# Optimization experiments

Hardware: AMD Instinct MI355X
Metric: run time of the kernel (lower is better)

Reference implementation:

```python
import jax, jax.numpy as jnp
import numpy as np
import math

H = 8
D_MODEL = 512
D_K = D_MODEL // H
NEG = -1.0e9


def setup_inputs() -> dict:
    key = jax.random.key(0)
    ks = jax.random.split(key, 10)
    B, S, D = 8, 1024, D_MODEL
    s = 1.0 / math.sqrt(D)
    return {
        "query": jax.random.normal(ks[0], (B, S, D), jnp.float32),
        "key": jax.random.normal(ks[1], (B, S, D), jnp.float32),
        "value": jax.random.normal(ks[2], (B, S, D), jnp.float32),
        "group_prob": jax.random.uniform(ks[3], (B, S, S), jnp.float32),
        "Wq": jax.random.normal(ks[4], (D, D), jnp.float32) * s,
        "Wk": jax.random.normal(ks[5], (D, D), jnp.float32) * s,
        "Wv": jax.random.normal(ks[6], (D, D), jnp.float32) * s,
        "Wh": jax.random.normal(ks[7], (D, D), jnp.float32) * s,
        "bh": jax.random.normal(ks[8], (D,), jnp.float32) * s,
        "mask": jax.random.randint(ks[9], (B, S, S), 0, 2, jnp.int32),
    }


def reference(query, key, value, group_prob, Wq, Wk, Wv, Wh, bh, mask):
    B, S, D = query.shape
    # project and split heads: [B, H, S, d_k]
    def split(x, W):
        return (x @ W.T).reshape(B, S, H, D_K).transpose(0, 2, 1, 3)
    q, k, v = split(query, Wq), split(key, Wk), split(value, Wv)
    scores = jnp.einsum('bhqd,bhkd->bhqk', q, k) / jnp.sqrt(jnp.asarray(D_K, q.dtype))
    # masked_fill where (mask | eye) == 0, i.e. keep mask-allowed or diagonal positions
    eye = jnp.eye(S, dtype=jnp.int32)
    allowed = (mask[:, None, :, :] | eye[None, None, :, :]) != 0  # [B,1,S,S]
    scores = jnp.where(allowed, scores, jnp.asarray(NEG, scores.dtype))
    p_attn = jax.nn.softmax(scores, axis=-1)
    p_attn = p_attn * group_prob[:, None, :, :]  # post-softmax group scaling
    x = jnp.einsum('bhqk,bhkd->bhqd', p_attn, v)
    x = x.transpose(0, 2, 1, 3).reshape(B, S, D)
    return x @ Wh.T + bh
```

## Files before the change

kernel.cpp:

```cpp
#include <hip/hip_runtime.h>
#include <hip/hip_bf16.h>
#include <cstdint>


typedef __attribute__((ext_vector_type(8))) short short8;
typedef __attribute__((ext_vector_type(4))) float f32x4;

__device__ __forceinline__ ushort f2bf(float x) {
    union { __hip_bfloat16 h; ushort u; } v;
    v.h = __float2bfloat16(x);
    return v.u;
}
__device__ __forceinline__ float bf2f(ushort u) {
    union { uint u; float f; } v; v.u = ((uint)u) << 16; return v.f;
}
__device__ __forceinline__ uint cvtpk(float lo, float hi) {
    uint r;
    asm("v_cvt_pk_bf16_f32 %0, %1, %2" : "=v"(r) : "v"(lo), "v"(hi));
    return r;
}
__device__ __forceinline__ f32x4 mfma16(short8 a, short8 b, f32x4 c) {
    return __builtin_amdgcn_mfma_f32_16x16x32_bf16(a, b, c, 0, 0, 0);
}
__device__ __forceinline__ void gl16(const void* g, const void* l) {
    __builtin_amdgcn_global_load_lds(
        (const __attribute__((address_space(1))) uint32_t*)(uintptr_t)g,
        (__attribute__((address_space(3))) uint32_t*)(uint32_t)(uintptr_t)l,
        16, 0, 0);
}

__global__ __launch_bounds__(256)
void prep(const float* __restrict__ q, const float* __restrict__ k,
          const float* __restrict__ v,
          const float* __restrict__ wq, const float* __restrict__ wk,
          const float* __restrict__ wv, const float* __restrict__ wh,
          const int* __restrict__ mask, const float* __restrict__ gp,
          ushort* __restrict__ qb, ushort* __restrict__ kb,
          ushort* __restrict__ vb,
          ushort* __restrict__ wqb, ushort* __restrict__ wkb,
          ushort* __restrict__ wvb, ushort* __restrict__ whb,
          ushort* __restrict__ gmb)
{
    const int bid = blockIdx.x, tid = threadIdx.x;
    if (bid < 8192) {
        size_t i = ((size_t)bid * 256 + tid) * 4;
        int4 m = *(const int4*)(mask + i);
        float4 gg = *(const float4*)(gp + i);
        int kk = (int)(i & 1023), qq = (int)((i >> 10) & 1023);
        uint u01 = cvtpk(gg.x, gg.y), u23 = cvtpk(gg.z, gg.w);
        ushort4 o;
        o.x = (m.x != 0 || qq == kk + 0) ? (ushort)(u01 & 0xffff) : (ushort)0xBF80;
        o.y = (m.y != 0 || qq == kk + 1) ? (ushort)(u01 >> 16)    : (ushort)0xBF80;
        o.z = (m.z != 0 || qq == kk + 2) ? (ushort)(u23 & 0xffff) : (ushort)0xBF80;
        o.w = (m.w != 0 || qq == kk + 3) ? (ushort)(u23 >> 16)    : (ushort)0xBF80;
        *(ushort4*)(gmb + i) = o;
    } else if (bid < 20480) {
        size_t id = ((size_t)(bid - 8192) * 256 + tid) * 4;
        int t = (int)(id >> 22);
        size_t off = id & 4194303;
        const float* s = (t == 0) ? q : (t == 1) ? k : v;
        ushort* d = (t == 0) ? qb : (t == 1) ? kb : vb;
        float4 x = *(const float4*)(s + off);
        uint2 o; o.x = cvtpk(x.x, x.y); o.y = cvtpk(x.z, x.w);
        *(uint2*)(d + off) = o;
    } else {
        size_t id = ((size_t)(bid - 20480) * 256 + tid) * 4;
        int t = (int)(id >> 18);
        size_t off = id & 262143;
        const float* s = (t == 0) ? wq : (t == 1) ? wk : (t == 2) ? wv : wh;
        ushort* d = (t == 0) ? wqb : (t == 1) ? wkb : (t == 2) ? wvb : whb;
        float4 x = *(const float4*)(s + off);
        uint2 o; o.x = cvtpk(x.x, x.y); o.y = cvtpk(x.z, x.w);
        *(uint2*)(d + off) = o;
    }
}

__global__ __launch_bounds__(256, 2)
void gemm3(const ushort* __restrict__ qb, const ushort* __restrict__ kb,
           const ushort* __restrict__ vb,
           const ushort* __restrict__ Wqb, const ushort* __restrict__ Wkb,
           const ushort* __restrict__ Wvb,
           ushort* __restrict__ q_ws, ushort* __restrict__ k_ws,
           ushort* __restrict__ vT)
{
    __shared__ __attribute__((aligned(16))) ushort As[8192];
    __shared__ __attribute__((aligned(16))) ushort Bs[8192];

    const int z = blockIdx.z;
    const ushort* A = (z == 0) ? qb : (z == 1) ? kb : Wvb;
    const ushort* B = (z == 0) ? Wqb : (z == 1) ? Wkb : vb;
    const int mt = (z == 2) ? blockIdx.y : blockIdx.x;
    const int nt = (z == 2) ? blockIdx.x : blockIdx.y;
    const int m0 = mt * 128, n0 = nt * 128;
    const int tid = threadIdx.x, lane = tid & 63, wave = tid >> 6;
    const int l15 = lane & 15, g = lane >> 4;
    const int wm = wave >> 1, wn = wave & 1;

    const int cb = (lane & 7) << 4;
    int soff[4];
    #pragma unroll
    for (int it = 0; it < 4; ++it) {
        int r = (it * 4 + wave) * 8 + (lane >> 3);
        soff[it] = r * 1024 + (cb ^ ((r & 7) << 4));
    }
    const char* Ab = (const char*)A + (size_t)m0 * 1024;
    const char* Bb = (const char*)B + (size_t)n0 * 1024;

    const int sw = (l15 & 7) << 4;
    const int c0 = (g * 16) ^ sw;
    const int c1 = (64 + g * 16) ^ sw;

    f32x4 acc[4][4];
    #pragma unroll
    for (int i = 0; i < 4; ++i)
        #pragma unroll
        for (int j = 0; j < 4; ++j) acc[i][j] = (f32x4){0.f, 0.f, 0.f, 0.f};

    for (int ks = 0; ks < 8; ++ks) {
        const int kof = ks * 128;
        #pragma unroll
        for (int it = 0; it < 4; ++it) {
            gl16(Ab + soff[it] + kof, (const char*)As + (it * 4 + wave) * 1024);
            gl16(Bb + soff[it] + kof, (const char*)Bs + (it * 4 + wave) * 1024);
        }
        __syncthreads();
        #pragma unroll
        for (int kk = 0; kk < 2; ++kk) {
            const int cc = kk ? c1 : c0;
            short8 af[4], bf[4];
            #pragma unroll
            for (int i = 0; i < 4; ++i)
                af[i] = *(const short8*)((const char*)As + (wm * 64 + i * 16 + l15) * 128 + cc);
            #pragma unroll
            for (int j = 0; j < 4; ++j)
                bf[j] = *(const short8*)((const char*)Bs + (wn * 64 + j * 16 + l15) * 128 + cc);
            #pragma unroll
            for (int i = 0; i < 4; ++i)
                #pragma unroll
                for (int j = 0; j < 4; ++j)
                    acc[i][j] = mfma16(af[i], bf[j], acc[i][j]);
        }
        __syncthreads();
    }

    #pragma unroll
    for (int i = 0; i < 4; ++i) {
        #pragma unroll
        for (int j = 0; j < 4; ++j) {
            #pragma unroll
            for (int r = 0; r < 4; ++r) {
                int mm = m0 + wm * 64 + i * 16 + g * 4 + r;
                int nn = n0 + wn * 64 + j * 16 + l15;
                float val = acc[i][j][r];
                if (z == 0) {
                    val *= 0.18033688f;
                    int b = mm >> 10, s = mm & 1023, h = nn >> 6, dk = nn & 63;
                    q_ws[((((size_t)(b * 8 + h)) << 10) + s) * 64 + dk] = f2bf(val);
                } else if (z == 1) {
                    int b = mm >> 10, s = mm & 1023, h = nn >> 6, dk = nn & 63;
                    k_ws[((((size_t)(b * 8 + h)) << 10) + s) * 64 + dk] = f2bf(val);
                } else {
                    int h = mm >> 6, d = mm & 63, b = nn >> 10, s = nn & 1023;
                    vT[(((size_t)(b * 8 + h) * 64 + d) << 10) + s] = f2bf(val);
                }
            }
        }
    }
}

__global__ __launch_bounds__(256, 2)
void gemm_o(const ushort* __restrict__ Xh, const ushort* __restrict__ Whb,
            const float* __restrict__ bias, float* __restrict__ out)
{
    __shared__ __attribute__((aligned(16))) ushort As[8192];
    __shared__ __attribute__((aligned(16))) ushort Bs[8192];

    const int m0 = blockIdx.x * 128, n0 = blockIdx.y * 128;
    const int tid = threadIdx.x, lane = tid & 63, wave = tid >> 6;
    const int l15 = lane & 15, g = lane >> 4;
    const int wm = wave >> 1, wn = wave & 1;
    const int bb = m0 >> 10, s0 = m0 & 1023;

    const int cb = (lane & 7) << 4;
    int aoff[4], boff[4];
    #pragma unroll
    for (int it = 0; it < 4; ++it) {
        int r = (it * 4 + wave) * 8 + (lane >> 3);
        int swz = cb ^ ((r & 7) << 4);
        aoff[it] = ((bb * 8) * 1024 + s0 + r) * 128 + swz;
        boff[it] = (n0 + r) * 1024 + swz;
    }
    const int sw = (l15 & 7) << 4;
    const int c0 = (g * 16) ^ sw;
    const int c1 = (64 + g * 16) ^ sw;

    f32x4 acc[4][4];
    #pragma unroll
    for (int i = 0; i < 4; ++i)
        #pragma unroll
        for (int j = 0; j < 4; ++j) acc[i][j] = (f32x4){0.f, 0.f, 0.f, 0.f};

    for (int ks = 0; ks < 8; ++ks) {
        #pragma unroll
        for (int it = 0; it < 4; ++it) {
            gl16((const char*)Xh + aoff[it] + ks * 131072,
                 (const char*)As + (it * 4 + wave) * 1024);
            gl16((const char*)Whb + boff[it] + ks * 128,
                 (const char*)Bs + (it * 4 + wave) * 1024);
        }
        __syncthreads();
        #pragma unroll
        for (int kk = 0; kk < 2; ++kk) {
            const int cc = kk ? c1 : c0;
            short8 af[4], bf[4];
            #pragma unroll
            for (int i = 0; i < 4; ++i)
                af[i] = *(const short8*)((const char*)As + (wm * 64 + i * 16 + l15) * 128 + cc);
            #pragma unroll
            for (int j = 0; j < 4; ++j)
                bf[j] = *(const short8*)((const char*)Bs + (wn * 64 + j * 16 + l15) * 128 + cc);
            #pragma unroll
            for (int i = 0; i < 4; ++i)
                #pragma unroll
                for (int j = 0; j < 4; ++j)
                    acc[i][j] = mfma16(af[i], bf[j], acc[i][j]);
        }
        __syncthreads();
    }

    float bv[4];
    #pragma unroll
    for (int j = 0; j < 4; ++j) bv[j] = bias[n0 + wn * 64 + j * 16 + l15];

    #pragma unroll
    for (int i = 0; i < 4; ++i)
        #pragma unroll
        for (int j = 0; j < 4; ++j)
            #pragma unroll
            for (int r = 0; r < 4; ++r) {
                int mm = m0 + wm * 64 + i * 16 + g * 4 + r;
                int nn = n0 + wn * 64 + j * 16 + l15;
                out[(size_t)mm * 512 + nn] = acc[i][j][r] + bv[j];
            }
}

__global__ __launch_bounds__(256, 2)
void attn(const ushort* __restrict__ Qh, const ushort* __restrict__ Kh,
          const ushort* __restrict__ Vt, const ushort* __restrict__ gm,
          ushort* __restrict__ xo)
{
    __shared__ __attribute__((aligned(16))) ushort kv[2][2][4096];

    const int w = blockIdx.x;
    const int bh = w & 63, qt = w >> 6;
    const int tid = threadIdx.x, wave = tid >> 6, lane = tid & 63;
    const int l15 = lane & 15, g = lane >> 4;
    const int q0 = qt * 128 + wave * 32;
    const int b = bh >> 3;

    const char* Kpb = (const char*)(Kh + (size_t)bh * 65536);
    const char* Vpb = (const char*)(Vt + (size_t)bh * 65536);
    const ushort* QpA = Qh + ((size_t)bh * 1024 + q0 + l15) * 64;
    const ushort* QpB = QpA + 16 * 64;
    const ushort* gmpA = gm + ((size_t)b * 1024 + q0 + l15) * 1024;
    const ushort* gmpB = gmpA + 16 * 1024;

    const short8 qa0 = *(const short8*)(QpA + g * 8);
    const short8 qa1 = *(const short8*)(QpA + 32 + g * 8);
    const short8 qb0 = *(const short8*)(QpB + g * 8);
    const short8 qb1 = *(const short8*)(QpB + 32 + g * 8);

    const int cb = (lane & 7) << 4;
    const int rA = wave * 8 + (lane >> 3);
    const int rB = rA + 32;
    const int gkA = (rA & 3) + 4 * ((rA >> 4) & 1) + 8 * ((rA >> 2) & 3) + 32 * (rA >> 5);
    const int gkB = (rB & 3) + 4 * ((rB >> 4) & 1) + 8 * ((rB >> 2) & 3) + 32 * (rB >> 5);
    const int okA = gkA * 128 + (cb ^ ((rA & 7) << 4));
    const int okB = gkB * 128 + (cb ^ ((rB & 7) << 4));
    const int ovA = rA * 2048 + (cb ^ ((rA & 7) << 4));
    const int ovB = rB * 2048 + (cb ^ ((rB & 7) << 4));

    const int sw = (l15 & 7) << 4;
    const int c0 = (g * 16) ^ sw;
    const int c1 = (64 + g * 16) ^ sw;

    f32x4 otA[4], otB[4];
    #pragma unroll
    for (int t = 0; t < 4; ++t) {
        otA[t] = (f32x4){0.f, 0.f, 0.f, 0.f};
        otB[t] = (f32x4){0.f, 0.f, 0.f, 0.f};
    }
    float lsA = 0.f, lsB = 0.f;

    gl16(Kpb + okA, &kv[0][0][wave * 512]);
    gl16(Kpb + okB, &kv[0][0][(4 + wave) * 512]);
    gl16(Vpb + ovA, &kv[0][1][wave * 512]);
    gl16(Vpb + ovB, &kv[0][1][(4 + wave) * 512]);
    short8 gcA0 = *(const short8*)(gmpA + g * 8);
    short8 gcA1 = *(const short8*)(gmpA + 32 + g * 8);
    short8 gcB0 = *(const short8*)(gmpB + g * 8);
    short8 gcB1 = *(const short8*)(gmpB + 32 + g * 8);
    __syncthreads();

    for (int t = 0; t < 16; ++t) {
        const int cur = t & 1;
        short8 gnA0, gnA1, gnB0, gnB1;
        if (t < 15) {
            const char* kp = Kpb + (size_t)(t + 1) * 8192;
            const char* vp = Vpb + (size_t)(t + 1) * 128;
            gl16(kp + okA, &kv[cur ^ 1][0][wave * 512]);
            gl16(kp + okB, &kv[cur ^ 1][0][(4 + wave) * 512]);
            gl16(vp + ovA, &kv[cur ^ 1][1][wave * 512]);
            gl16(vp + ovB, &kv[cur ^ 1][1][(4 + wave) * 512]);
            gnA0 = *(const short8*)(gmpA + (t + 1) * 64 + g * 8);
            gnA1 = *(const short8*)(gmpA + (t + 1) * 64 + 32 + g * 8);
            gnB0 = *(const short8*)(gmpB + (t + 1) * 64 + g * 8);
            gnB1 = *(const short8*)(gmpB + (t + 1) * 64 + 32 + g * 8);
        }
        const char* kbuf = (const char*)&kv[cur][0][0];
        const char* vbuf = (const char*)&kv[cur][1][0];

        f32x4 sA[4], sB[4];
        #pragma unroll
        for (int t4 = 0; t4 < 4; ++t4) {
            const char* ka = kbuf + (t4 * 16 + l15) * 128;
            short8 k0f = *(const short8*)(ka + c0);
            short8 k1f = *(const short8*)(ka + c1);
            f32x4 za = (f32x4){0.f, 0.f, 0.f, 0.f};
            za = mfma16(k0f, qa0, za);
            za = mfma16(k1f, qa1, za);
            sA[t4] = za;
            f32x4 zb = (f32x4){0.f, 0.f, 0.f, 0.f};
            zb = mfma16(k0f, qb0, zb);
            zb = mfma16(k1f, qb1, zb);
            sB[t4] = zb;
        }

        union { uint4 u; short8 s; } paA0, paA1, paB0, paB1;
        {
            float p[16], gv[16];
            #pragma unroll
            for (int c = 0; c < 2; ++c) {
                const short8 gc = c ? gcA1 : gcA0;
                #pragma unroll
                for (int j = 0; j < 8; ++j) {
                    const int jj = c * 8 + j;
                    const int t4 = 2 * c + (j >> 2), r = j & 3;
                    float gvv = bf2f((ushort)gc[j]);
                    gv[jj] = gvv;
                    p[jj] = exp2f((gvv >= 0.f) ? sA[t4][r] : -1.0e9f);
                }
            }
            lsA += (((p[0] + p[1]) + (p[2] + p[3])) + ((p[4] + p[5]) + (p[6] + p[7])))
                 + (((p[8] + p[9]) + (p[10] + p[11])) + ((p[12] + p[13]) + (p[14] + p[15])));
            paA0.u.x = cvtpk(p[0] * gv[0],  p[1] * gv[1]);
            paA0.u.y = cvtpk(p[2] * gv[2],  p[3] * gv[3]);
            paA0.u.z = cvtpk(p[4] * gv[4],  p[5] * gv[5]);
            paA0.u.w = cvtpk(p[6] * gv[6],  p[7] * gv[7]);
            paA1.u.x = cvtpk(p[8] * gv[8],  p[9] * gv[9]);
            paA1.u.y = cvtpk(p[10] * gv[10], p[11] * gv[11]);
            paA1.u.z = cvtpk(p[12] * gv[12], p[13] * gv[13]);
            paA1.u.w = cvtpk(p[14] * gv[14], p[15] * gv[15]);
        }
        {
            float p[16], gv[16];
            #pragma unroll
            for (int c = 0; c < 2; ++c) {
                const short8 gc = c ? gcB1 : gcB0;
                #pragma unroll
                for (int j = 0; j < 8; ++j) {
                    const int jj = c * 8 + j;
                    const int t4 = 2 * c + (j >> 2), r = j & 3;
                    float gvv = bf2f((ushort)gc[j]);
                    gv[jj] = gvv;
                    p[jj] = exp2f((gvv >= 0.f) ? sB[t4][r] : -1.0e9f);
                }
            }
            lsB += (((p[0] + p[1]) + (p[2] + p[3])) + ((p[4] + p[5]) + (p[6] + p[7])))
                 + (((p[8] + p[9]) + (p[10] + p[11])) + ((p[12] + p[13]) + (p[14] + p[15])));
            paB0.u.x = cvtpk(p[0] * gv[0],  p[1] * gv[1]);
            paB0.u.y = cvtpk(p[2] * gv[2],  p[3] * gv[3]);
            paB0.u.z = cvtpk(p[4] * gv[4],  p[5] * gv[5]);
            paB0.u.w = cvtpk(p[6] * gv[6],  p[7] * gv[7]);
            paB1.u.x = cvtpk(p[8] * gv[8],  p[9] * gv[9]);
            paB1.u.y = cvtpk(p[10] * gv[10], p[11] * gv[11]);
            paB1.u.z = cvtpk(p[12] * gv[12], p[13] * gv[13]);
            paB1.u.w = cvtpk(p[14] * gv[14], p[15] * gv[15]);
        }

        #pragma unroll
        for (int td = 0; td < 4; ++td) {
            const char* va = vbuf + (td * 16 + l15) * 128;
            short8 v0 = *(const short8*)(va + c0);
            short8 v1 = *(const short8*)(va + c1);
            otA[td] = mfma16(v0, paA0.s, otA[td]);
            otA[td] = mfma16(v1, paA1.s, otA[td]);
            otB[td] = mfma16(v0, paB0.s, otB[td]);
            otB[td] = mfma16(v1, paB1.s, otB[td]);
        }
        __syncthreads();
        if (t < 15) { gcA0 = gnA0; gcA1 = gnA1; gcB0 = gnB0; gcB1 = gnB1; }
    }

    lsA += __shfl_xor(lsA, 16, 64);
    lsA += __shfl_xor(lsA, 32, 64);
    lsB += __shfl_xor(lsB, 16, 64);
    lsB += __shfl_xor(lsB, 32, 64);
    const float invA = 1.0f / lsA;
    const float invB = 1.0f / lsB;

    ushort* xpA = xo + ((size_t)bh * 1024 + q0 + l15) * 64;
    ushort* xpB = xpA + 16 * 64;
    #pragma unroll
    for (int td = 0; td < 4; ++td) {
        uint2 oa, ob;
        oa.x = cvtpk(otA[td][0] * invA, otA[td][1] * invA);
        oa.y = cvtpk(otA[td][2] * invA, otA[td][3] * invA);
        ob.x = cvtpk(otB[td][0] * invB, otB[td][1] * invB);
        ob.y = cvtpk(otB[td][2] * invB, otB[td][3] * invB);
        *(uint2*)(xpA + td * 16 + g * 4) = oa;
        *(uint2*)(xpB + td * 16 + g * 4) = ob;
    }
}

extern "C" void kernel_launch(void* const* d_in, const int* in_sizes, int n_in,
                              void* d_out, int out_size, void* d_ws, size_t ws_size,
                              hipStream_t stream)
{
    const float* query = (const float*)d_in[0];
    const float* key   = (const float*)d_in[1];
    const float* value = (const float*)d_in[2];
    const float* gprob = (const float*)d_in[3];
    const float* Wq    = (const float*)d_in[4];
    const float* Wk    = (const float*)d_in[5];
    const float* Wv    = (const float*)d_in[6];
    const float* Wh    = (const float*)d_in[7];
    const float* bh    = (const float*)d_in[8];
    const int*   mask  = (const int*)d_in[9];
    float* out = (float*)d_out;

    ushort* ws = (ushort*)d_ws;
    const size_t HS = (size_t)64 * 65536;
    ushort* q_ws = ws;
    ushort* k_ws = ws + HS;
    ushort* vT   = ws + 2 * HS;
    ushort* gmb  = ws + 3 * HS;
    ushort* qb   = ws + 5 * HS;
    ushort* kb   = ws + 6 * HS;
    ushort* vb   = ws + 7 * HS;
    ushort* wqb  = ws + 8 * HS;
    ushort* wkb  = wqb + 262144;
    ushort* wvb  = wkb + 262144;
    ushort* whb  = wvb + 262144;
    ushort* x_ws = qb;

    prep<<<21504, 256, 0, stream>>>(query, key, value, Wq, Wk, Wv, Wh,
                                    mask, gprob, qb, kb, vb,
                                    wqb, wkb, wvb, whb, gmb);
    gemm3<<<dim3(64, 4, 3), 256, 0, stream>>>(qb, kb, vb, wqb, wkb, wvb,
                                              q_ws, k_ws, vT);
    attn<<<512, 256, 0, stream>>>(q_ws, k_ws, vT, gmb, x_ws);
    gemm_o<<<dim3(64, 4), 256, 0, stream>>>(x_ws, whb, bh, out);
}
```

Before: 101.8 us.

## Halve attention block size and hand-schedule double-buffered KV loads with explicit waitcnt

The attention kernel now runs 2 waves per block (64 queries) across twice as many blocks. Each wave loads 4 K and 4 V chunks, and the tile loop is unrolled by two so the ping-pong buffer index is a compile-time constant. __syncthreads is replaced with an explicit vmcnt wait plus raw s_barrier, so the next tile's prefetch stays in flight. setprio raises wave priority around the MFMA sections. Each block now loads K/V for only 64 queries, so K/V global traffic per query doubles, traded for finer blocks and better latency hiding.

```diff
diff --git a/kernel.cpp b/kernel.cpp
--- a/kernel.cpp
+++ b/kernel.cpp
@@ -244,7 +244,97 @@
             }
 }
 
-__global__ __launch_bounds__(256, 2)
+__device__ __forceinline__ void softmax16(const short8 gc0, const short8 gc1,
+                                          const f32x4 (&s4)[4], float& lsum,
+                                          uint4& u0, uint4& u1)
+{
+    float p[16], gv[16];
+    #pragma unroll
+    for (int c = 0; c < 2; ++c) {
+        const short8 gc = c ? gc1 : gc0;
+        #pragma unroll
+        for (int j = 0; j < 8; ++j) {
+            const int jj = c * 8 + j;
+            const int t4 = 2 * c + (j >> 2), r = j & 3;
+            float gvv = bf2f((ushort)gc[j]);
+            gv[jj] = gvv;
+            p[jj] = exp2f((gvv >= 0.f) ? s4[t4][r] : -1.0e9f);
+        }
+    }
+    lsum += (((p[0] + p[1]) + (p[2] + p[3])) + ((p[4] + p[5]) + (p[6] + p[7])))
+          + (((p[8] + p[9]) + (p[10] + p[11])) + ((p[12] + p[13]) + (p[14] + p[15])));
+    u0.x = cvtpk(p[0] * gv[0],  p[1] * gv[1]);
+    u0.y = cvtpk(p[2] * gv[2],  p[3] * gv[3]);
+    u0.z = cvtpk(p[4] * gv[4],  p[5] * gv[5]);
+    u0.w = cvtpk(p[6] * gv[6],  p[7] * gv[7]);
+    u1.x = cvtpk(p[8] * gv[8],  p[9] * gv[9]);
+    u1.y = cvtpk(p[10] * gv[10], p[11] * gv[11]);
+    u1.z = cvtpk(p[12] * gv[12], p[13] * gv[13]);
+    u1.w = cvtpk(p[14] * gv[14], p[15] * gv[15]);
+}
+
+#define TILE_BODY(T, CUR, GCA0, GCA1, GCB0, GCB1, GNA0, GNA1, GNB0, GNB1)      \
+  do {                                                                         \
+    if ((T) < 15) {                                                            \
+        GNA0 = *(const short8*)(gmpA + ((T) + 1) * 64 + g * 8);                \
+        GNA1 = *(const short8*)(gmpA + ((T) + 1) * 64 + 32 + g * 8);           \
+        GNB0 = *(const short8*)(gmpB + ((T) + 1) * 64 + g * 8);                \
+        GNB1 = *(const short8*)(gmpB + ((T) + 1) * 64 + 32 + g * 8);           \
+        const char* kp_ = Kpb + (size_t)((T) + 1) * 8192;                      \
+        const char* vp_ = Vpb + (size_t)((T) + 1) * 128;                       \
+        char* kd_ = (char*)&kv[(CUR) ^ 1][0][0] + wave * 4096;                 \
+        char* vd_ = (char*)&kv[(CUR) ^ 1][1][0] + wave * 4096;                 \
+        _Pragma("unroll")                                                      \
+        for (int i_ = 0; i_ < 4; ++i_) {                                       \
+            gl16(kp_ + koff[i_], kd_ + i_ * 1024);                             \
+            gl16(vp_ + voff[i_], vd_ + i_ * 1024);                             \
+        }                                                                      \
+        asm volatile("s_waitcnt vmcnt(12)" ::: "memory");                      \
+    } else {                                                                   \
+        asm volatile("s_waitcnt vmcnt(0)" ::: "memory");                       \
+    }                                                                          \
+    __builtin_amdgcn_s_barrier();                                              \
+    __builtin_amdgcn_sched_barrier(0);                                         \
+    {                                                                          \
+        const char* kbuf_ = (const char*)&kv[CUR][0][0];                       \
+        const char* vbuf_ = (const char*)&kv[CUR][1][0];                       \
+        f32x4 sA_[4], sB_[4];                                                  \
+        __builtin_amdgcn_s_setprio(1);                                         \
+        _Pragma("unroll")                                                      \
+        for (int t4_ = 0; t4_ < 4; ++t4_) {                                    \
+            const char* ka_ = kbuf_ + (t4_ * 16 + l15) * 128;                  \
+            short8 k0_ = *(const short8*)(ka_ + c0);                           \
+            short8 k1_ = *(const short8*)(ka_ + c1);                           \
+            f32x4 za_ = (f32x4){0.f, 0.f, 0.f, 0.f};                           \
+            za_ = mfma16(k0_, qa0, za_);                                       \
+            za_ = mfma16(k1_, qa1, za_);                                       \
+            sA_[t4_] = za_;                                                    \
+            f32x4 zb_ = (f32x4){0.f, 0.f, 0.f, 0.f};                           \
+            zb_ = mfma16(k0_, qb0, zb_);                                       \
+            zb_ = mfma16(k1_, qb1, zb_);                                       \
+            sB_[t4_] = zb_;                                                    \
+        }                                                                      \
+        __builtin_amdgcn_s_setprio(0);                                         \
+        union { uint4 u; short8 s; } paA0_, paA1_, paB0_, paB1_;               \
+        softmax16(GCA0, GCA1, sA_, lsA, paA0_.u, paA1_.u);                     \
+        softmax16(GCB0, GCB1, sB_, lsB, paB0_.u, paB1_.u);                     \
+        __builtin_amdgcn_s_setprio(1);                                         \
+        _Pragma("unroll")                                                      \
+        for (int td_ = 0; td_ < 4; ++td_) {                                    \
+            const char* va_ = vbuf_ + (td_ * 16 + l15) * 128;                  \
+            short8 v0_ = *(const short8*)(va_ + c0);                           \
+            short8 v1_ = *(const short8*)(va_ + c1);                           \
+            otA[td_] = mfma16(v0_, paA0_.s, otA[td_]);                         \
+            otA[td_] = mfma16(v1_, paA1_.s, otA[td_]);                         \
+            otB[td_] = mfma16(v0_, paB0_.s, otB[td_]);                         \
+            otB[td_] = mfma16(v1_, paB1_.s, otB[td_]);                         \
+        }                                                                      \
+        __builtin_amdgcn_s_setprio(0);                                         \
+    }                                                                          \
+    __builtin_amdgcn_s_barrier();                                              \
+  } while (0)
+
+__global__ __launch_bounds__(128, 2)
 void attn(const ushort* __restrict__ Qh, const ushort* __restrict__ Kh,
           const ushort* __restrict__ Vt, const ushort* __restrict__ gm,
           ushort* __restrict__ xo)
@@ -255,30 +345,30 @@
     const int bh = w & 63, qt = w >> 6;
     const int tid = threadIdx.x, wave = tid >> 6, lane = tid & 63;
     const int l15 = lane & 15, g = lane >> 4;
-    const int q0 = qt * 128 + wave * 32;
+    const int q0 = qt * 64 + wave * 32;
     const int b = bh >> 3;
 
     const char* Kpb = (const char*)(Kh + (size_t)bh * 65536);
     const char* Vpb = (const char*)(Vt + (size_t)bh * 65536);
     const ushort* QpA = Qh + ((size_t)bh * 1024 + q0 + l15) * 64;
-    const ushort* QpB = QpA + 16 * 64;
+    const ushort* QpB = QpA + 1024;
     const ushort* gmpA = gm + ((size_t)b * 1024 + q0 + l15) * 1024;
-    const ushort* gmpB = gmpA + 16 * 1024;
+    const ushort* gmpB = gmpA + 16384;
 
     const short8 qa0 = *(const short8*)(QpA + g * 8);
     const short8 qa1 = *(const short8*)(QpA + 32 + g * 8);
     const short8 qb0 = *(const short8*)(QpB + g * 8);
     const short8 qb1 = *(const short8*)(QpB + 32 + g * 8);
 
-    const int cb = (lane & 7) << 4;
-    const int rA = wave * 8 + (lane >> 3);
-    const int rB = rA + 32;
-    const int gkA = (rA & 3) + 4 * ((rA >> 4) & 1) + 8 * ((rA >> 2) & 3) + 32 * (rA >> 5);
-    const int gkB = (rB & 3) + 4 * ((rB >> 4) & 1) + 8 * ((rB >> 2) & 3) + 32 * (rB >> 5);
-    const int okA = gkA * 128 + (cb ^ ((rA & 7) << 4));
-    const int okB = gkB * 128 + (cb ^ ((rB & 7) << 4));
-    const int ovA = rA * 2048 + (cb ^ ((rA & 7) << 4));
-    const int ovB = rB * 2048 + (cb ^ ((rB & 7) << 4));
+    const int cbk = ((lane & 7) << 4) ^ ((lane >> 3) << 4);
+    int koff[4], voff[4];
+    #pragma unroll
+    for (int i = 0; i < 4; ++i) {
+        int p = (wave * 4 + i) * 8 + (lane >> 3);
+        int gk = (p & 3) + 4 * ((p >> 4) & 1) + 8 * ((p >> 2) & 3) + 32 * (p >> 5);
+        koff[i] = gk * 128 + cbk;
+        voff[i] = p * 2048 + cbk;
+    }
 
     const int sw = (l15 & 7) << 4;
     const int c0 = (g * 16) ^ sw;
@@ -292,114 +382,24 @@
     }
     float lsA = 0.f, lsB = 0.f;
 
-    gl16(Kpb + okA, &kv[0][0][wave * 512]);
-    gl16(Kpb + okB, &kv[0][0][(4 + wave) * 512]);
-    gl16(Vpb + ovA, &kv[0][1][wave * 512]);
-    gl16(Vpb + ovB, &kv[0][1][(4 + wave) * 512]);
-    short8 gcA0 = *(const short8*)(gmpA + g * 8);
-    short8 gcA1 = *(const short8*)(gmpA + 32 + g * 8);
-    short8 gcB0 = *(const short8*)(gmpB + g * 8);
-    short8 gcB1 = *(const short8*)(gmpB + 32 + g * 8);
-    __syncthreads();
-
-    for (int t = 0; t < 16; ++t) {
-        const int cur = t & 1;
-        short8 gnA0, gnA1, gnB0, gnB1;
-        if (t < 15) {
-            const char* kp = Kpb + (size_t)(t + 1) * 8192;
-            const char* vp = Vpb + (size_t)(t + 1) * 128;
-            gl16(kp + okA, &kv[cur ^ 1][0][wave * 512]);
-            gl16(kp + okB, &kv[cur ^ 1][0][(4 + wave) * 512]);
-            gl16(vp + ovA, &kv[cur ^ 1][1][wave * 512]);
-            gl16(vp + ovB, &kv[cur ^ 1][1][(4 + wave) * 512]);
-            gnA0 = *(const short8*)(gmpA + (t + 1) * 64 + g * 8);
-            gnA1 = *(const short8*)(gmpA + (t + 1) * 64 + 32 + g * 8);
-            gnB0 = *(const short8*)(gmpB + (t + 1) * 64 + g * 8);
-            gnB1 = *(const short8*)(gmpB + (t + 1) * 64 + 32 + g * 8);
-        }
-        const char* kbuf = (const char*)&kv[cur][0][0];
-        const char* vbuf = (const char*)&kv[cur][1][0];
-
-        f32x4 sA[4], sB[4];
-        #pragma unroll
-        for (int t4 = 0; t4 < 4; ++t4) {
-            const char* ka = kbuf + (t4 * 16 + l15) * 128;
-            short8 k0f = *(const short8*)(ka + c0);
-            short8 k1f = *(const short8*)(ka + c1);
-            f32x4 za = (f32x4){0.f, 0.f, 0.f, 0.f};
-            za = mfma16(k0f, qa0, za);
-            za = mfma16(k1f, qa1, za);
-            sA[t4] = za;
-            f32x4 zb = (f32x4){0.f, 0.f, 0.f, 0.f};
-            zb = mfma16(k0f, qb0, zb);
-            zb = mfma16(k1f, qb1, zb);
-            sB[t4] = zb;
-        }
-
-        union { uint4 u; short8 s; } paA0, paA1, paB0, paB1;
-        {
-            float p[16], gv[16];
-            #pragma unroll
-            for (int c = 0; c < 2; ++c) {
-                const short8 gc = c ? gcA1 : gcA0;
-                #pragma unroll
-                for (int j = 0; j < 8; ++j) {
-                    const int jj = c * 8 + j;
-                    const int t4 = 2 * c + (j >> 2), r = j & 3;
-                    float gvv = bf2f((ushort)gc[j]);
-                    gv[jj] = gvv;
-                    p[jj] = exp2f((gvv >= 0.f) ? sA[t4][r] : -1.0e9f);
-                }
-            }
-            lsA += (((p[0] + p[1]) + (p[2] + p[3])) + ((p[4] + p[5]) + (p[6] + p[7])))
-                 + (((p[8] + p[9]) + (p[10] + p[11])) + ((p[12] + p[13]) + (p[14] + p[15])));
-            paA0.u.x = cvtpk(p[0] * gv[0],  p[1] * gv[1]);
-            paA0.u.y = cvtpk(p[2] * gv[2],  p[3] * gv[3]);
-            paA0.u.z = cvtpk(p[4] * gv[4],  p[5] * gv[5]);
-            paA0.u.w = cvtpk(p[6] * gv[6],  p[7] * gv[7]);
-            paA1.u.x = cvtpk(p[8] * gv[8],  p[9] * gv[9]);
-            paA1.u.y = cvtpk(p[10] * gv[10], p[11] * gv[11]);
-            paA1.u.z = cvtpk(p[12] * gv[12], p[13] * gv[13]);
-            paA1.u.w = cvtpk(p[14] * gv[14], p[15] * gv[15]);
-        }
-        {
-            float p[16], gv[16];
-            #pragma unroll
-            for (int c = 0; c < 2; ++c) {
-                const short8 gc = c ? gcB1 : gcB0;
-                #pragma unroll
-                for (int j = 0; j < 8; ++j) {
-                    const int jj = c * 8 + j;
-                    const int t4 = 2 * c + (j >> 2), r = j & 3;
-                    float gvv = bf2f((ushort)gc[j]);
-                    gv[jj] = gvv;
-                    p[jj] = exp2f((gvv >= 0.f) ? sB[t4][r] : -1.0e9f);
-                }
-            }
-            lsB += (((p[0] + p[1]) + (p[2] + p[3])) + ((p[4] + p[5]) + (p[6] + p[7])))
-                 + (((p[8] + p[9]) + (p[10] + p[11])) + ((p[12] + p[13]) + (p[14] + p[15])));
-            paB0.u.x = cvtpk(p[0] * gv[0],  p[1] * gv[1]);
-            paB0.u.y = cvtpk(p[2] * gv[2],  p[3] * gv[3]);
-            paB0.u.z = cvtpk(p[4] * gv[4],  p[5] * gv[5]);
-            paB0.u.w = cvtpk(p[6] * gv[6],  p[7] * gv[7]);
-            paB1.u.x = cvtpk(p[8] * gv[8],  p[9] * gv[9]);
-            paB1.u.y = cvtpk(p[10] * gv[10], p[11] * gv[11]);
-            paB1.u.z = cvtpk(p[12] * gv[12], p[13] * gv[13]);
-            paB1.u.w = cvtpk(p[14] * gv[14], p[15] * gv[15]);
-        }
-
-        #pragma unroll
-        for (int td = 0; td < 4; ++td) {
-            const char* va = vbuf + (td * 16 + l15) * 128;
-            short8 v0 = *(const short8*)(va + c0);
-            short8 v1 = *(const short8*)(va + c1);
-            otA[td] = mfma16(v0, paA0.s, otA[td]);
-            otA[td] = mfma16(v1, paA1.s, otA[td]);
-            otB[td] = mfma16(v0, paB0.s, otB[td]);
-            otB[td] = mfma16(v1, paB1.s, otB[td]);
-        }
-        __syncthreads();
-        if (t < 15) { gcA0 = gnA0; gcA1 = gnA1; gcB0 = gnB0; gcB1 = gnB1; }
+    short8 gEA0 = *(const short8*)(gmpA + g * 8);
+    short8 gEA1 = *(const short8*)(gmpA + 32 + g * 8);
+    short8 gEB0 = *(const short8*)(gmpB + g * 8);
+    short8 gEB1 = *(const short8*)(gmpB + 32 + g * 8);
+    short8 gOA0, gOA1, gOB0, gOB1;
+    {
+        char* kd = (char*)&kv[0][0][0] + wave * 4096;
+        char* vd = (char*)&kv[0][1][0] + wave * 4096;
+        #pragma unroll
+        for (int i = 0; i < 4; ++i) {
+            gl16(Kpb + koff[i], kd + i * 1024);
+            gl16(Vpb + voff[i], vd + i * 1024);
+        }
+    }
+
+    for (int tt = 0; tt < 16; tt += 2) {
+        TILE_BODY(tt,     0, gEA0, gEA1, gEB0, gEB1, gOA0, gOA1, gOB0, gOB1);
+        TILE_BODY(tt + 1, 1, gOA0, gOA1, gOB0, gOB1, gEA0, gEA1, gEB0, gEB1);
     }
 
     lsA += __shfl_xor(lsA, 16, 64);
@@ -410,7 +410,7 @@
     const float invB = 1.0f / lsB;
 
     ushort* xpA = xo + ((size_t)bh * 1024 + q0 + l15) * 64;
-    ushort* xpB = xpA + 16 * 64;
+    ushort* xpB = xpA + 1024;
     #pragma unroll
     for (int td = 0; td < 4; ++td) {
         uint2 oa, ob;
@@ -459,6 +459,6 @@
                                     wqb, wkb, wvb, whb, gmb);
     gemm3<<<dim3(64, 4, 3), 256, 0, stream>>>(qb, kb, vb, wqb, wkb, wvb,
                                               q_ws, k_ws, vT);
-    attn<<<512, 256, 0, stream>>>(q_ws, k_ws, vT, gmb, x_ws);
+    attn<<<1024, 128, 0, stream>>>(q_ws, k_ws, vT, gmb, x_ws);
     gemm_o<<<dim3(64, 4), 256, 0, stream>>>(x_ws, whb, bh, out);
 }
```

New measurement: 104.8 us. 1.03x slower.

## Split attention key range across two wave groups with LDS reduction

Applied to the files above, without the earlier changes.

The attention kernel now launches 512 threads per block and splits the 1024-key sequence into two halves, each handled by a group of four waves with its own double-buffered K/V tiles in a 64KB LDS buffer. Partial outputs and row sums from the second half are written to LDS and combined by the first group before normalisation and the bf16 store. This doubles the waves available per block to hide latency of the serial key loop, at the cost of more LDS per block, a final reduction and synchronisation step, and launch bounds that may limit register use. The softmax code is also moved into a helper function.

```diff
diff --git a/kernel.cpp b/kernel.cpp
--- a/kernel.cpp
+++ b/kernel.cpp
@@ -244,41 +244,83 @@
             }
 }
 
-__global__ __launch_bounds__(256, 2)
+__device__ __forceinline__ void softmax16(const short8 gc0, const short8 gc1,
+                                          const f32x4 (&s4)[4], float& lsum,
+                                          uint4& u0, uint4& u1)
+{
+    float p[16], gv[16];
+    #pragma unroll
+    for (int c = 0; c < 2; ++c) {
+        const short8 gc = c ? gc1 : gc0;
+        #pragma unroll
+        for (int j = 0; j < 8; ++j) {
+            const int jj = c * 8 + j;
+            const int t4 = 2 * c + (j >> 2), r = j & 3;
+            float gvv = bf2f((ushort)gc[j]);
+            gv[jj] = gvv;
+            p[jj] = exp2f((gvv >= 0.f) ? s4[t4][r] : -1.0e9f);
+        }
+    }
+    lsum += (((p[0] + p[1]) + (p[2] + p[3])) + ((p[4] + p[5]) + (p[6] + p[7])))
+          + (((p[8] + p[9]) + (p[10] + p[11])) + ((p[12] + p[13]) + (p[14] + p[15])));
+    u0.x = cvtpk(p[0] * gv[0],  p[1] * gv[1]);
+    u0.y = cvtpk(p[2] * gv[2],  p[3] * gv[3]);
+    u0.z = cvtpk(p[4] * gv[4],  p[5] * gv[5]);
+    u0.w = cvtpk(p[6] * gv[6],  p[7] * gv[7]);
+    u1.x = cvtpk(p[8] * gv[8],  p[9] * gv[9]);
+    u1.y = cvtpk(p[10] * gv[10], p[11] * gv[11]);
+    u1.z = cvtpk(p[12] * gv[12], p[13] * gv[13]);
+    u1.w = cvtpk(p[14] * gv[14], p[15] * gv[15]);
+}
+
+__global__ __launch_bounds__(512, 4)
 void attn(const ushort* __restrict__ Qh, const ushort* __restrict__ Kh,
           const ushort* __restrict__ Vt, const ushort* __restrict__ gm,
           ushort* __restrict__ xo)
 {
-    __shared__ __attribute__((aligned(16))) ushort kv[2][2][4096];
+    __shared__ __attribute__((aligned(16))) char lds[65536];
 
     const int w = blockIdx.x;
     const int bh = w & 63, qt = w >> 6;
     const int tid = threadIdx.x, wave = tid >> 6, lane = tid & 63;
     const int l15 = lane & 15, g = lane >> 4;
-    const int q0 = qt * 128 + wave * 32;
+    const int ks = wave >> 2, wq = wave & 3;
+    const int q0 = qt * 128 + wq * 32;
     const int b = bh >> 3;
 
-    const char* Kpb = (const char*)(Kh + (size_t)bh * 65536);
-    const char* Vpb = (const char*)(Vt + (size_t)bh * 65536);
+    const char* Kpb = (const char*)(Kh + (size_t)bh * 65536) + ks * 65536;
+    const char* Vpb = (const char*)(Vt + (size_t)bh * 65536) + ks * 1024;
     const ushort* QpA = Qh + ((size_t)bh * 1024 + q0 + l15) * 64;
-    const ushort* QpB = QpA + 16 * 64;
-    const ushort* gmpA = gm + ((size_t)b * 1024 + q0 + l15) * 1024;
-    const ushort* gmpB = gmpA + 16 * 1024;
+    const ushort* QpB = QpA + 1024;
+    const ushort* gma  = gm + ((size_t)b * 1024 + q0 + l15) * 1024 + ks * 512 + g * 8;
+    const ushort* gmb2 = gma + 16384;
 
     const short8 qa0 = *(const short8*)(QpA + g * 8);
     const short8 qa1 = *(const short8*)(QpA + 32 + g * 8);
     const short8 qb0 = *(const short8*)(QpB + g * 8);
     const short8 qb1 = *(const short8*)(QpB + 32 + g * 8);
 
-    const int cb = (lane & 7) << 4;
-    const int rA = wave * 8 + (lane >> 3);
-    const int rB = rA + 32;
-    const int gkA = (rA & 3) + 4 * ((rA >> 4) & 1) + 8 * ((rA >> 2) & 3) + 32 * (rA >> 5);
-    const int gkB = (rB & 3) + 4 * ((rB >> 4) & 1) + 8 * ((rB >> 2) & 3) + 32 * (rB >> 5);
-    const int okA = gkA * 128 + (cb ^ ((rA & 7) << 4));
-    const int okB = gkB * 128 + (cb ^ ((rB & 7) << 4));
-    const int ovA = rA * 2048 + (cb ^ ((rA & 7) << 4));
-    const int ovB = rB * 2048 + (cb ^ ((rB & 7) << 4));
+    const int cbs = ((lane & 7) << 4) ^ ((lane >> 3) << 4);
+    const char* sbase;
+    int soff[4], doff[4], sstep;
+    if (wq < 2) {
+        sstep = 8192; sbase = Kpb;
+        #pragma unroll
+        for (int i = 0; i < 4; ++i) {
+            int r = (wq * 4 + i) * 8 + (lane >> 3);
+            int gk = (r & 3) + 4 * ((r >> 4) & 1) + 8 * ((r >> 2) & 3) + 32 * (r >> 5);
+            soff[i] = gk * 128 + cbs;
+            doff[i] = ks * 16384 + (wq * 4 + i) * 1024 + lane * 16;
+        }
+    } else {
+        sstep = 128; sbase = Vpb;
+        #pragma unroll
+        for (int i = 0; i < 4; ++i) {
+            int rv = ((wq - 2) * 4 + i) * 8 + (lane >> 3);
+            soff[i] = rv * 2048 + cbs;
+            doff[i] = ks * 16384 + 8192 + ((wq - 2) * 4 + i) * 1024 + lane * 16;
+        }
+    }
 
     const int sw = (l15 & 7) << 4;
     const int c0 = (g * 16) ^ sw;
@@ -292,33 +334,29 @@
     }
     float lsA = 0.f, lsB = 0.f;
 
-    gl16(Kpb + okA, &kv[0][0][wave * 512]);
-    gl16(Kpb + okB, &kv[0][0][(4 + wave) * 512]);
-    gl16(Vpb + ovA, &kv[0][1][wave * 512]);
-    gl16(Vpb + ovB, &kv[0][1][(4 + wave) * 512]);
-    short8 gcA0 = *(const short8*)(gmpA + g * 8);
-    short8 gcA1 = *(const short8*)(gmpA + 32 + g * 8);
-    short8 gcB0 = *(const short8*)(gmpB + g * 8);
-    short8 gcB1 = *(const short8*)(gmpB + 32 + g * 8);
+    #pragma unroll
+    for (int i = 0; i < 4; ++i) gl16(sbase + soff[i], lds + doff[i]);
+    short8 gcA0 = *(const short8*)(gma);
+    short8 gcA1 = *(const short8*)(gma + 32);
+    short8 gcB0 = *(const short8*)(gmb2);
+    short8 gcB1 = *(const short8*)(gmb2 + 32);
     __syncthreads();
 
-    for (int t = 0; t < 16; ++t) {
+    for (int t = 0; t < 8; ++t) {
         const int cur = t & 1;
         short8 gnA0, gnA1, gnB0, gnB1;
-        if (t < 15) {
-            const char* kp = Kpb + (size_t)(t + 1) * 8192;
-            const char* vp = Vpb + (size_t)(t + 1) * 128;
-            gl16(kp + okA, &kv[cur ^ 1][0][wave * 512]);
-            gl16(kp + okB, &kv[cur ^ 1][0][(4 + wave) * 512]);
-            gl16(vp + ovA, &kv[cur ^ 1][1][wave * 512]);
-            gl16(vp + ovB, &kv[cur ^ 1][1][(4 + wave) * 512]);
-            gnA0 = *(const short8*)(gmpA + (t + 1) * 64 + g * 8);
-            gnA1 = *(const short8*)(gmpA + (t + 1) * 64 + 32 + g * 8);
-            gnB0 = *(const short8*)(gmpB + (t + 1) * 64 + g * 8);
-            gnB1 = *(const short8*)(gmpB + (t + 1) * 64 + 32 + g * 8);
-        }
-        const char* kbuf = (const char*)&kv[cur][0][0];
-        const char* vbuf = (const char*)&kv[cur][1][0];
+        if (t < 7) {
+            #pragma unroll
+            for (int i = 0; i < 4; ++i)
+                gl16(sbase + (t + 1) * sstep + soff[i],
+                     lds + (cur ^ 1) * 32768 + doff[i]);
+            gnA0 = *(const short8*)(gma + (t + 1) * 64);
+            gnA1 = *(const short8*)(gma + (t + 1) * 64 + 32);
+            gnB0 = *(const short8*)(gmb2 + (t + 1) * 64);
+            gnB1 = *(const short8*)(gmb2 + (t + 1) * 64 + 32);
+        }
+        const char* kbuf = lds + cur * 32768 + ks * 16384;
+        const char* vbuf = kbuf + 8192;
 
         f32x4 sA[4], sB[4];
         #pragma unroll
@@ -337,56 +375,8 @@
         }
 
         union { uint4 u; short8 s; } paA0, paA1, paB0, paB1;
-        {
-            float p[16], gv[16];
-            #pragma unroll
-            for (int c = 0; c < 2; ++c) {
-                const short8 gc = c ? gcA1 : gcA0;
-                #pragma unroll
-                for (int j = 0; j < 8; ++j) {
-                    const int jj = c * 8 + j;
-                    const int t4 = 2 * c + (j >> 2), r = j & 3;
-                    float gvv = bf2f((ushort)gc[j]);
-                    gv[jj] = gvv;
-                    p[jj] = exp2f((gvv >= 0.f) ? sA[t4][r] : -1.0e9f);
-                }
-            }
-            lsA += (((p[0] + p[1]) + (p[2] + p[3])) + ((p[4] + p[5]) + (p[6] + p[7])))
-                 + (((p[8] + p[9]) + (p[10] + p[11])) + ((p[12] + p[13]) + (p[14] + p[15])));
-            paA0.u.x = cvtpk(p[0] * gv[0],  p[1] * gv[1]);
-            paA0.u.y = cvtpk(p[2] * gv[2],  p[3] * gv[3]);
-            paA0.u.z = cvtpk(p[4] * gv[4],  p[5] * gv[5]);
-            paA0.u.w = cvtpk(p[6] * gv[6],  p[7] * gv[7]);
-            paA1.u.x = cvtpk(p[8] * gv[8],  p[9] * gv[9]);
-            paA1.u.y = cvtpk(p[10] * gv[10], p[11] * gv[11]);
-            paA1.u.z = cvtpk(p[12] * gv[12], p[13] * gv[13]);
-            paA1.u.w = cvtpk(p[14] * gv[14], p[15] * gv[15]);
-        }
-        {
-            float p[16], gv[16];
-            #pragma unroll
-            for (int c = 0; c < 2; ++c) {
-                const short8 gc = c ? gcB1 : gcB0;
-                #pragma unroll
-                for (int j = 0; j < 8; ++j) {
-                    const int jj = c * 8 + j;
-                    const int t4 = 2 * c + (j >> 2), r = j & 3;
-                    float gvv = bf2f((ushort)gc[j]);
-                    gv[jj] = gvv;
-                    p[jj] = exp2f((gvv >= 0.f) ? sB[t4][r] : -1.0e9f);
-                }
-            }
-            lsB += (((p[0] + p[1]) + (p[2] + p[3])) + ((p[4] + p[5]) + (p[6] + p[7])))
-                 + (((p[8] + p[9]) + (p[10] + p[11])) + ((p[12] + p[13]) + (p[14] + p[15])));
-            paB0.u.x = cvtpk(p[0] * gv[0],  p[1] * gv[1]);
-            paB0.u.y = cvtpk(p[2] * gv[2],  p[3] * gv[3]);
-            paB0.u.z = cvtpk(p[4] * gv[4],  p[5] * gv[5]);
-            paB0.u.w = cvtpk(p[6] * gv[6],  p[7] * gv[7]);
-            paB1.u.x = cvtpk(p[8] * gv[8],  p[9] * gv[9]);
-            paB1.u.y = cvtpk(p[10] * gv[10], p[11] * gv[11]);
-            paB1.u.z = cvtpk(p[12] * gv[12], p[13] * gv[13]);
-            paB1.u.w = cvtpk(p[14] * gv[14], p[15] * gv[15]);
-        }
+        softmax16(gcA0, gcA1, sA, lsA, paA0.u, paA1.u);
+        softmax16(gcB0, gcB1, sB, lsB, paB0.u, paB1.u);
 
         #pragma unroll
         for (int td = 0; td < 4; ++td) {
@@ -399,27 +389,49 @@
             otB[td] = mfma16(v1, paB1.s, otB[td]);
         }
         __syncthreads();
-        if (t < 15) { gcA0 = gnA0; gcA1 = gnA1; gcB0 = gnB0; gcB1 = gnB1; }
+        if (t < 7) { gcA0 = gnA0; gcA1 = gnA1; gcB0 = gnB0; gcB1 = gnB1; }
     }
 
     lsA += __shfl_xor(lsA, 16, 64);
     lsA += __shfl_xor(lsA, 32, 64);
     lsB += __shfl_xor(lsB, 16, 64);
     lsB += __shfl_xor(lsB, 32, 64);
-    const float invA = 1.0f / lsA;
-    const float invB = 1.0f / lsB;
-
-    ushort* xpA = xo + ((size_t)bh * 1024 + q0 + l15) * 64;
-    ushort* xpB = xpA + 16 * 64;
-    #pragma unroll
-    for (int td = 0; td < 4; ++td) {
-        uint2 oa, ob;
-        oa.x = cvtpk(otA[td][0] * invA, otA[td][1] * invA);
-        oa.y = cvtpk(otA[td][2] * invA, otA[td][3] * invA);
-        ob.x = cvtpk(otB[td][0] * invB, otB[td][1] * invB);
-        ob.y = cvtpk(otB[td][2] * invB, otB[td][3] * invB);
-        *(uint2*)(xpA + td * 16 + g * 4) = oa;
-        *(uint2*)(xpB + td * 16 + g * 4) = ob;
+
+    float* mO = (float*)lds;
+    float* mL = (float*)(lds + 32768);
+    if (ks == 1) {
+        float* dA = mO + wq * 2048 + l15 * 64;
+        float* dB = mO + wq * 2048 + (l15 + 16) * 64;
+        #pragma unroll
+        for (int td = 0; td < 4; ++td) {
+            *(f32x4*)(dA + td * 16 + g * 4) = otA[td];
+            *(f32x4*)(dB + td * 16 + g * 4) = otB[td];
+        }
+        if (g == 0) {
+            mL[wq * 32 + l15] = lsA;
+            mL[wq * 32 + 16 + l15] = lsB;
+        }
+    }
+    __syncthreads();
+    if (ks == 0) {
+        const float invA = 1.0f / (lsA + mL[wq * 32 + l15]);
+        const float invB = 1.0f / (lsB + mL[wq * 32 + 16 + l15]);
+        const float* dA = mO + wq * 2048 + l15 * 64;
+        const float* dB = mO + wq * 2048 + (l15 + 16) * 64;
+        ushort* xpA = xo + ((size_t)bh * 1024 + q0 + l15) * 64;
+        ushort* xpB = xpA + 1024;
+        #pragma unroll
+        for (int td = 0; td < 4; ++td) {
+            f32x4 a2 = *(const f32x4*)(dA + td * 16 + g * 4);
+            f32x4 b2 = *(const f32x4*)(dB + td * 16 + g * 4);
+            uint2 oa, ob;
+            oa.x = cvtpk((otA[td][0] + a2[0]) * invA, (otA[td][1] + a2[1]) * invA);
+            oa.y = cvtpk((otA[td][2] + a2[2]) * invA, (otA[td][3] + a2[3]) * invA);
+            ob.x = cvtpk((otB[td][0] + b2[0]) * invB, (otB[td][1] + b2[1]) * invB);
+            ob.y = cvtpk((otB[td][2] + b2[2]) * invB, (otB[td][3] + b2[3]) * invB);
+            *(uint2*)(xpA + td * 16 + g * 4) = oa;
+            *(uint2*)(xpB + td * 16 + g * 4) = ob;
+        }
     }
 }
 
@@ -459,6 +471,6 @@
                                     wqb, wkb, wvb, whb, gmb);
     gemm3<<<dim3(64, 4, 3), 256, 0, stream>>>(qb, kb, vb, wqb, wkb, wvb,
                                               q_ws, k_ws, vT);
-    attn<<<512, 256, 0, stream>>>(q_ws, k_ws, vT, gmb, x_ws);
+    attn<<<512, 512, 0, stream>>>(q_ws, k_ws, vT, gmb, x_ws);
     gemm_o<<<dim3(64, 4), 256, 0, stream>>>(x_ws, whb, bh, out);
 }
```

Measured after the change: 106.1 us. +4.3%, slower.

## Move mask/group-prob packing into the projection GEMM launch to overlap them

Applied to the files above, without the earlier changes.

Removes the mask and group_prob packing from the prep kernel and runs it in extra blocks of the QKV projection GEMM launch, now a flattened 1D grid. The memory-bound packing blocks are meant to overlap with the compute-bound GEMM blocks instead of running serially before them. The extra blocks each handle four strided chunks. This adds block-scheduling interplay, and the GEMM blocks could be slowed by competing bandwidth.

```diff
diff --git a/kernel.cpp b/kernel.cpp
--- a/kernel.cpp
+++ b/kernel.cpp
@@ -34,28 +34,14 @@
           const float* __restrict__ v,
           const float* __restrict__ wq, const float* __restrict__ wk,
           const float* __restrict__ wv, const float* __restrict__ wh,
-          const int* __restrict__ mask, const float* __restrict__ gp,
           ushort* __restrict__ qb, ushort* __restrict__ kb,
           ushort* __restrict__ vb,
           ushort* __restrict__ wqb, ushort* __restrict__ wkb,
-          ushort* __restrict__ wvb, ushort* __restrict__ whb,
-          ushort* __restrict__ gmb)
+          ushort* __restrict__ wvb, ushort* __restrict__ whb)
 {
     const int bid = blockIdx.x, tid = threadIdx.x;
-    if (bid < 8192) {
-        size_t i = ((size_t)bid * 256 + tid) * 4;
-        int4 m = *(const int4*)(mask + i);
-        float4 gg = *(const float4*)(gp + i);
-        int kk = (int)(i & 1023), qq = (int)((i >> 10) & 1023);
-        uint u01 = cvtpk(gg.x, gg.y), u23 = cvtpk(gg.z, gg.w);
-        ushort4 o;
-        o.x = (m.x != 0 || qq == kk + 0) ? (ushort)(u01 & 0xffff) : (ushort)0xBF80;
-        o.y = (m.y != 0 || qq == kk + 1) ? (ushort)(u01 >> 16)    : (ushort)0xBF80;
-        o.z = (m.z != 0 || qq == kk + 2) ? (ushort)(u23 & 0xffff) : (ushort)0xBF80;
-        o.w = (m.w != 0 || qq == kk + 3) ? (ushort)(u23 >> 16)    : (ushort)0xBF80;
-        *(ushort4*)(gmb + i) = o;
-    } else if (bid < 20480) {
-        size_t id = ((size_t)(bid - 8192) * 256 + tid) * 4;
+    if (bid < 12288) {
+        size_t id = ((size_t)bid * 256 + tid) * 4;
         int t = (int)(id >> 22);
         size_t off = id & 4194303;
         const float* s = (t == 0) ? q : (t == 1) ? k : v;
@@ -64,7 +50,7 @@
         uint2 o; o.x = cvtpk(x.x, x.y); o.y = cvtpk(x.z, x.w);
         *(uint2*)(d + off) = o;
     } else {
-        size_t id = ((size_t)(bid - 20480) * 256 + tid) * 4;
+        size_t id = ((size_t)(bid - 12288) * 256 + tid) * 4;
         int t = (int)(id >> 18);
         size_t off = id & 262143;
         const float* s = (t == 0) ? wq : (t == 1) ? wk : (t == 2) ? wv : wh;
@@ -76,23 +62,47 @@
 }
 
 __global__ __launch_bounds__(256, 2)
-void gemm3(const ushort* __restrict__ qb, const ushort* __restrict__ kb,
-           const ushort* __restrict__ vb,
-           const ushort* __restrict__ Wqb, const ushort* __restrict__ Wkb,
-           const ushort* __restrict__ Wvb,
-           ushort* __restrict__ q_ws, ushort* __restrict__ k_ws,
-           ushort* __restrict__ vT)
+void fused_g(const ushort* __restrict__ qb, const ushort* __restrict__ kb,
+             const ushort* __restrict__ vb,
+             const ushort* __restrict__ Wqb, const ushort* __restrict__ Wkb,
+             const ushort* __restrict__ Wvb,
+             const int* __restrict__ mask, const float* __restrict__ gp,
+             ushort* __restrict__ q_ws, ushort* __restrict__ k_ws,
+             ushort* __restrict__ vT, ushort* __restrict__ gmb)
 {
     __shared__ __attribute__((aligned(16))) ushort As[8192];
     __shared__ __attribute__((aligned(16))) ushort Bs[8192];
 
-    const int z = blockIdx.z;
+    const int bid = blockIdx.x, tid = threadIdx.x;
+
+    if (bid >= 768) {
+        const size_t base = ((size_t)(bid - 768) * 256 + tid) * 4;
+        #pragma unroll
+        for (int s = 0; s < 4; ++s) {
+            size_t i = base + (size_t)s * 2097152;
+            int4 m = *(const int4*)(mask + i);
+            float4 gg = *(const float4*)(gp + i);
+            int kk = (int)(i & 1023), qq = (int)((i >> 10) & 1023);
+            uint u01 = cvtpk(gg.x, gg.y), u23 = cvtpk(gg.z, gg.w);
+            ushort4 o;
+            o.x = (m.x != 0 || qq == kk + 0) ? (ushort)(u01 & 0xffff) : (ushort)0xBF80;
+            o.y = (m.y != 0 || qq == kk + 1) ? (ushort)(u01 >> 16)    : (ushort)0xBF80;
+            o.z = (m.z != 0 || qq == kk + 2) ? (ushort)(u23 & 0xffff) : (ushort)0xBF80;
+            o.w = (m.w != 0 || qq == kk + 3) ? (ushort)(u23 >> 16)    : (ushort)0xBF80;
+            *(ushort4*)(gmb + i) = o;
+        }
+        return;
+    }
+
+    const int z = bid >> 8;
+    const int tt2 = bid & 255;
+    const int mt0 = tt2 >> 2, nt0 = tt2 & 3;
     const ushort* A = (z == 0) ? qb : (z == 1) ? kb : Wvb;
     const ushort* B = (z == 0) ? Wqb : (z == 1) ? Wkb : vb;
-    const int mt = (z == 2) ? blockIdx.y : blockIdx.x;
-    const int nt = (z == 2) ? blockIdx.x : blockIdx.y;
+    const int mt = (z == 2) ? nt0 : mt0;
+    const int nt = (z == 2) ? mt0 : nt0;
     const int m0 = mt * 128, n0 = nt * 128;
-    const int tid = threadIdx.x, lane = tid & 63, wave = tid >> 6;
+    const int lane = tid & 63, wave = tid >> 6;
     const int l15 = lane & 15, g = lane >> 4;
     const int wm = wave >> 1, wn = wave & 1;
 
@@ -454,11 +464,10 @@
     ushort* whb  = wvb + 262144;
     ushort* x_ws = qb;
 
-    prep<<<21504, 256, 0, stream>>>(query, key, value, Wq, Wk, Wv, Wh,
-                                    mask, gprob, qb, kb, vb,
-                                    wqb, wkb, wvb, whb, gmb);
-    gemm3<<<dim3(64, 4, 3), 256, 0, stream>>>(qb, kb, vb, wqb, wkb, wvb,
-                                              q_ws, k_ws, vT);
+    prep<<<13312, 256, 0, stream>>>(query, key, value, Wq, Wk, Wv, Wh,
+                                    qb, kb, vb, wqb, wkb, wvb, whb);
+    fused_g<<<2816, 256, 0, stream>>>(qb, kb, vb, wqb, wkb, wvb,
+                                      mask, gprob, q_ws, k_ws, vT, gmb);
     attn<<<512, 256, 0, stream>>>(q_ws, k_ws, vT, gmb, x_ws);
     gemm_o<<<dim3(64, 4), 256, 0, stream>>>(x_ws, whb, bh, out);
 }
```

Result: slower. 105.4 us (+3.6%).
